# Performance work log

Hardware: AMD Instinct MI355X
Metric: run time of the kernel (lower is better)

## Reference

```python
import jax, jax.numpy as jnp
import numpy as np

N, DIM, HEADS, E = 20000, 256, 4, 100000
C = DIM  # TransformerConv out_channels per head (concat=False averages heads)


def setup_inputs() -> dict:
    key = jax.random.key(0)
    ks = jax.random.split(key, 12)
    s = DIM ** -0.5
    w = lambda k, shape: jax.random.normal(k, shape, jnp.float32) * s
    z = lambda shape: jnp.zeros(shape, jnp.float32)
    return {
        "f_all": jax.random.normal(ks[0], (N, DIM), jnp.float32),
        "edge_index": jax.random.randint(ks[1], (2, E), 0, N),
        "W_gcn": w(ks[2], (DIM, DIM)), "b_gcn": z((DIM,)),
        "W_q": w(ks[3], (DIM, HEADS * C)), "b_q": z((HEADS * C,)),
        "W_k": w(ks[4], (DIM, HEADS * C)), "b_k": z((HEADS * C,)),
        "W_v": w(ks[5], (DIM, HEADS * C)), "b_v": z((HEADS * C,)),
        "W_skip": w(ks[6], (DIM, DIM)), "b_skip": z((DIM,)),
        "W_beta": w(ks[7], (3 * DIM, 1)),
        "W_cnn": w(ks[8], (DIM, DIM)), "b_cnn": z((DIM,)),
    }


def reference(f_all, edge_index, W_gcn, b_gcn, W_q, b_q, W_k, b_k, W_v, b_v,
              W_skip, b_skip, W_beta, W_cnn, b_cnn):
    src, dst = edge_index[0], edge_index[1]

    # --- GCNConv: add self loops, symmetric D^-1/2 (A+I) D^-1/2 normalization ---
    loop = jnp.arange(N)
    s2 = jnp.concatenate([src, loop])
    d2 = jnp.concatenate([dst, loop])
    deg = jax.ops.segment_sum(jnp.ones_like(d2, jnp.float32), d2, N)
    dinv = jnp.where(deg > 0, 1.0 / jnp.sqrt(deg), 0.0)
    norm = dinv[s2] * dinv[d2]                    # [E+N]
    h = f_all @ W_gcn                             # [N, DIM]
    x = jax.ops.segment_sum(h[s2] * norm[:, None], d2, N) + b_gcn
    x = jax.nn.relu(x)

    # --- TransformerConv(heads=H, concat=False, beta=True) ---
    q = (x @ W_q + b_q).reshape(N, HEADS, C)
    k = (x @ W_k + b_k).reshape(N, HEADS, C)
    v = (x @ W_v + b_v).reshape(N, HEADS, C)
    logits = jnp.einsum('ehc,ehc->eh', q[dst], k[src]) / np.float32(np.sqrt(C))
    m = jax.ops.segment_max(logits, dst, N)       # per-target max for stable softmax
    e = jnp.exp(logits - m[dst])
    denom = jax.ops.segment_sum(e, dst, N)
    alpha = e / jnp.maximum(denom[dst], 1e-16)    # [E, H]
    agg = jax.ops.segment_sum(v[src] * alpha[:, :, None], dst, N)  # [N, H, C]
    out = agg.mean(axis=1)                        # concat=False -> head average
    xr = x @ W_skip + b_skip                      # root/skip branch
    beta = jax.nn.sigmoid(jnp.concatenate([out, xr, out - xr], axis=-1) @ W_beta)
    tf = jax.nn.relu(beta * xr + (1.0 - beta) * out)  # [N, DIM]

    # --- Conv1d with kernel (dim,1) on [1,1,dim,N]: per-node linear, output [dim,N] ---
    conv = jnp.einsum('cd,nd->cn', W_cnn, tf) + b_cnn[:, None]  # [DIM, N]
    # torch does .view(1, n_mole, -1) on the [1,dim,1,N] conv output: raw reshape
    return conv.reshape(1, N, DIM)
```

## Files before the change

### kernel.cpp

```cpp
#include <hip/hip_runtime.h>
#include <math.h>

#define DIMC 256
#define NHEAD 4
#define CAP 64

typedef unsigned short bf16u;
typedef __attribute__((ext_vector_type(8))) short bf16x8;
typedef __attribute__((ext_vector_type(4))) float f32x4;

typedef __attribute__((address_space(1))) const unsigned char ga_u8;
typedef __attribute__((address_space(3))) unsigned char lds_u8;
__device__ __forceinline__ void gld_lds16(const void* g, void* l) {
    __builtin_amdgcn_global_load_lds((ga_u8*)g, (lds_u8*)l, 16, 0, 0);
}

__device__ __forceinline__ float bf2f(bf16u u) {
    union { float f; unsigned int i; } c; c.i = ((unsigned int)u) << 16; return c.f;
}
__device__ __forceinline__ bf16u f2bf(float f) {
    union { float f; unsigned int i; } c; c.f = f;
    unsigned int r = c.i + 0x7fffu + ((c.i >> 16) & 1u);
    return (bf16u)(r >> 16);
}
__device__ __forceinline__ float4 load_bf4(const bf16u* p) {
    ushort4 raw = *(const ushort4*)p;
    return make_float4(bf2f(raw.x), bf2f(raw.y), bf2f(raw.z), bf2f(raw.w));
}
__device__ __forceinline__ void store_bf4(bf16u* p, float4 v) {
    ushort4 raw;
    raw.x = f2bf(v.x); raw.y = f2bf(v.y); raw.z = f2bf(v.z); raw.w = f2bf(v.w);
    *(ushort4*)p = raw;
}
__device__ __forceinline__ void load_bf8(const bf16u* p, float* o) {
    bf16x8 raw = *(const bf16x8*)p;
#pragma unroll
    for (int i = 0; i < 8; ++i) {
        union { float f; unsigned int u; } c;
        c.u = ((unsigned int)(unsigned short)raw[i]) << 16;
        o[i] = c.f;
    }
}
__device__ __forceinline__ void store_bf8(bf16u* p, const float* v) {
    bf16x8 raw;
#pragma unroll
    for (int i = 0; i < 8; ++i) raw[i] = (short)f2bf(v[i]);
    *(bf16x8*)p = raw;
}


__global__ void fill_kernel(const int* __restrict__ src, const int* __restrict__ dst,
                            int* __restrict__ cursor, int* __restrict__ srcs, int E) {
    int e = blockIdx.x * 256 + threadIdx.x;
    if (e < E) {
        int d = dst[e];
        int pos = atomicAdd(&cursor[d], 1);
        if (pos < CAP) srcs[d * CAP + pos] = src[e];
    }
}


__global__ __launch_bounds__(256) void prep_kernel(
    const float* __restrict__ f_all, int n4_f,
    const float* __restrict__ W_gcn, const float* __restrict__ W_q,
    const float* __restrict__ W_k, const float* __restrict__ W_v,
    const float* __restrict__ W_skip, const float* __restrict__ W_cnn,
    const float* __restrict__ b_q, const float* __restrict__ b_v,
    const float* __restrict__ b_skip,
    bf16u* __restrict__ xbuf, bf16u* __restrict__ WgcnT,
    bf16u* __restrict__ BTyp, bf16u* __restrict__ BT_vs,
    bf16u* __restrict__ A_wq, bf16u* __restrict__ A_wk,
    bf16u* __restrict__ Wcnn_b,
    float* __restrict__ ybias, float* __restrict__ bvm,
    int* __restrict__ cursor, int N) {
    __shared__ float T[32][33];
    int b = blockIdx.x, t = threadIdx.x;
    int nf = (n4_f + 255) >> 8;
    int nz = (N + 255) >> 8;
    if (b < nf) {
        int i = b * 256 + t;
        if (i < n4_f) {
            float4 vv = *(const float4*)(f_all + (size_t)i * 4);
            store_bf4(xbuf + (size_t)i * 4, vv);
        }
        return;
    }
    b -= nf;
    if (b < 64) {
        int i = b * 256 + t;
        float4 vv = *(const float4*)(W_cnn + (size_t)i * 4);
        store_bf4(Wcnn_b + (size_t)i * 4, vv);
        return;
    }
    b -= 64;
    if (b < 4) {
        int h = b, j = t;
        const float4* bq4 = (const float4*)(b_q + h * 256);
        const float4* wk4 = (const float4*)(W_k + (size_t)j * 1024 + h * 256);
        float acc = 0.f;
        for (int u = 0; u < 64; ++u) {
            float4 a = bq4[u], w = wk4[u];
            acc += a.x * w.x + a.y * w.y + a.z * w.z + a.w * w.w;
        }
        ybias[h * 256 + j] = acc;
        return;
    }
    b -= 4;
    if (b < 1) {
        ybias[1024 + t] = b_skip[t];
        bvm[t] = 0.25f * (b_v[t] + b_v[256 + t] + b_v[512 + t] + b_v[768 + t]);
        return;
    }
    b -= 1;
    if (b < nz) {
        int i = b * 256 + t;
        if (i < N) cursor[i] = 0;
        return;
    }
    b -= nz;
    if (b < 512) {
        const float* W = (b < 256) ? W_q : W_k;
        bf16u* out = (b < 256) ? A_wq : A_wk;
        int i4 = (b & 255) * 256 + t;
        int e = i4 * 4;
        int g = e >> 8, t4 = e & 255;
        float4 vv = *(const float4*)(W + (size_t)(g & 255) * 1024 + (g >> 8) * 256 + t4);
        store_bf4(out + (size_t)e, vv);
        return;
    }
    b -= 512;
    const float* src; bf16u* dst;
    int inld, inrow0, incol0, outld, outrow0, outcol0;
    if (b < 64) {
        int N0 = (b & 7) * 32, K0 = (b >> 3) * 32;
        src = W_gcn; inld = 256; inrow0 = K0; incol0 = N0;
        dst = WgcnT; outld = 256; outrow0 = N0; outcol0 = K0;
    } else if (b < 128) {
        int bb = b - 64; int N0 = (bb & 7) * 32, K0 = (bb >> 3) * 32;
        src = W_skip; inld = 256; inrow0 = K0; incol0 = N0;
        dst = BTyp;  outld = 256; outrow0 = 1024 + N0; outcol0 = K0;
    } else {
        int bb = b - 128; int jt = bb & 7, ct = (bb >> 3) & 7, hh = bb >> 6;
        src = W_v;  inld = 1024; inrow0 = ct * 32; incol0 = hh * 256 + jt * 32;
        dst = BT_vs; outld = 1024; outrow0 = jt * 32; outcol0 = hh * 256 + ct * 32;
    }
    int tx = t & 31, ty = t >> 5;
#pragma unroll
    for (int i = 0; i < 4; ++i)
        T[ty + 8 * i][tx] = src[(size_t)(inrow0 + ty + 8 * i) * inld + incol0 + tx];
    __syncthreads();
#pragma unroll
    for (int i = 0; i < 4; ++i)
        dst[(size_t)(outrow0 + ty + 8 * i) * outld + outcol0 + tx] = f2bf(T[tx][ty + 8 * i]);
}


template <bool ROWBIAS>
__global__ __launch_bounds__(256) void gemm_tile(const bf16u* __restrict__ A,
                                                 const bf16u* __restrict__ BT,
                                                 const float* __restrict__ bias,
                                                 void* __restrict__ Cout,
                                                 int M, int Nc, int ldc, int K,
                                                 int zstrA, int zstrB, int zstrC) {
    __shared__ __align__(16) bf16u As[2][128][32];
    __shared__ __align__(16) bf16u Bs[2][128][32];
    A += (size_t)blockIdx.z * zstrA;
    BT += (size_t)blockIdx.z * zstrB;
    int t = threadIdx.x;
    int w = t >> 6, lane = t & 63;
    int q = lane >> 4, r = lane & 15;
    int wm = (w & 1) * 64, wn = (w >> 1) * 64;
    int bm = blockIdx.y * 128, bn = blockIdx.x * 128;

    int srow = t >> 2, scol = (t & 3) * 8;
    int arow0 = bm + srow;      if (arow0 >= M)  arow0 = M - 1;
    int arow1 = bm + 64 + srow; if (arow1 >= M)  arow1 = M - 1;
    int brow0 = bn + srow;      if (brow0 >= Nc) brow0 = Nc - 1;
    int brow1 = bn + 64 + srow; if (brow1 >= Nc) brow1 = Nc - 1;
    const bf16u* a0 = A + (size_t)arow0 * K + scol;
    const bf16u* a1 = A + (size_t)arow1 * K + scol;
    const bf16u* b0 = BT + (size_t)brow0 * K + scol;
    const bf16u* b1 = BT + (size_t)brow1 * K + scol;

    char* As_base = (char*)&As[0][0][0] + w * 1024;
    char* Bs_base = (char*)&Bs[0][0][0] + w * 1024;

    f32x4 acc[4][4] = {};
    int ngroups = K >> 6;
    for (int g = 0; g < ngroups; ++g) {
        int k0 = g * 64;
        gld_lds16(a0 + k0, As_base);
        gld_lds16(a1 + k0, As_base + 4096);
        gld_lds16(b0 + k0, Bs_base);
        gld_lds16(b1 + k0, Bs_base + 4096);
        gld_lds16(a0 + k0 + 32, As_base + 8192);
        gld_lds16(a1 + k0 + 32, As_base + 8192 + 4096);
        gld_lds16(b0 + k0 + 32, Bs_base + 8192);
        gld_lds16(b1 + k0 + 32, Bs_base + 8192 + 4096);
        __syncthreads();
#pragma unroll
        for (int ks = 0; ks < 2; ++ks) {
            bf16x8 af[4], bfr[4];
#pragma unroll
            for (int i = 0; i < 4; ++i) af[i] = *(const bf16x8*)&As[ks][wm + i * 16 + r][q * 8];
#pragma unroll
            for (int j = 0; j < 4; ++j) bfr[j] = *(const bf16x8*)&Bs[ks][wn + j * 16 + r][q * 8];
#pragma unroll
            for (int i = 0; i < 4; ++i)
#pragma unroll
                for (int j = 0; j < 4; ++j)
                    acc[i][j] = __builtin_amdgcn_mfma_f32_16x16x32_bf16(af[i], bfr[j], acc[i][j], 0, 0, 0);
        }
        __syncthreads();
    }

    if (ROWBIAS) {
        float* C = (float*)Cout + (size_t)blockIdx.z * zstrC;
#pragma unroll
        for (int j = 0; j < 4; ++j) {
            int col = bn + wn + j * 16 + r;
            if (col >= Nc) continue;
#pragma unroll
            for (int i = 0; i < 4; ++i)
#pragma unroll
                for (int rg = 0; rg < 4; ++rg) {
                    int row = bm + wm + i * 16 + q * 4 + rg;
                    if (row < M)
                        __builtin_nontemporal_store(acc[i][j][rg] + bias[row],
                                                    &C[(size_t)row * ldc + col]);
                }
        }
    } else {
        __shared__ __align__(16) bf16u Cs[32][128];
        bf16u* C = (bf16u*)Cout + (size_t)blockIdx.z * zstrC;
        float cb4[4];
#pragma unroll
        for (int j = 0; j < 4; ++j) {
            int col = bn + wn + j * 16 + r;
            cb4[j] = bias ? bias[col] : 0.0f;
        }
        int rhalf = (w & 1) * 16;
        int colbase = (w >> 1) * 64;
        __syncthreads();
#pragma unroll
        for (int i = 0; i < 4; ++i) {
#pragma unroll
            for (int j = 0; j < 4; ++j)
#pragma unroll
                for (int rg = 0; rg < 4; ++rg)
                    Cs[rhalf + q * 4 + rg][colbase + j * 16 + r] = f2bf(acc[i][j][rg] + cb4[j]);
            __syncthreads();
#pragma unroll
            for (int cpass = 0; cpass < 2; ++cpass) {
                int chunk = cpass * 256 + t;
                int sr = chunk >> 4;
                int c16 = chunk & 15;
                int grow = bm + (sr < 16 ? i * 16 + sr : 64 + i * 16 + (sr - 16));
                if (grow < M)
                    __builtin_nontemporal_store(*(const bf16x8*)&Cs[sr][c16 * 8],
                                                (bf16x8*)&C[(size_t)grow * ldc + bn + c16 * 8]);
            }
            __syncthreads();
        }
    }
}


__global__ __launch_bounds__(256) void gcn_agg_kernel(const bf16u* __restrict__ h,
                                                      const int* __restrict__ cursor,
                                                      const int* __restrict__ srcs,
                                                      const float* __restrict__ b_gcn,
                                                      bf16u* __restrict__ x, int N) {
    int n = blockIdx.x * 8 + (threadIdx.x >> 5);
    if (n >= N) return;
    int lane = threadIdx.x & 31;
    int cb = lane * 8;
    int cnt = cursor[n]; if (cnt > CAP) cnt = CAP;
    float dn = rsqrtf((float)(cnt + 1));
    float hn[8];
    load_bf8(h + (size_t)n * DIMC + cb, hn);
    int base = n * CAP;
    float acc[8] = {};
    int i = 0;
    for (; i + 4 <= cnt; i += 4) {
        int4 s4 = *(const int4*)(srcs + base + i);
        float d0 = rsqrtf((float)(cursor[s4.x] + 1));
        float d1 = rsqrtf((float)(cursor[s4.y] + 1));
        float d2 = rsqrtf((float)(cursor[s4.z] + 1));
        float d3 = rsqrtf((float)(cursor[s4.w] + 1));
        float h0[8], h1[8], h2[8], h3[8];
        load_bf8(h + (size_t)s4.x * DIMC + cb, h0);
        load_bf8(h + (size_t)s4.y * DIMC + cb, h1);
        load_bf8(h + (size_t)s4.z * DIMC + cb, h2);
        load_bf8(h + (size_t)s4.w * DIMC + cb, h3);
#pragma unroll
        for (int j = 0; j < 8; ++j)
            acc[j] += h0[j] * d0 + h1[j] * d1 + h2[j] * d2 + h3[j] * d3;
    }
    for (; i < cnt; ++i) {
        int s = srcs[base + i];
        float ds = rsqrtf((float)(cursor[s] + 1));
        float hv[8];
        load_bf8(h + (size_t)s * DIMC + cb, hv);
#pragma unroll
        for (int j = 0; j < 8; ++j) acc[j] += hv[j] * ds;
    }
    float4 bg0 = *(const float4*)(b_gcn + cb);
    float4 bg1 = *(const float4*)(b_gcn + cb + 4);
    float bg[8] = {bg0.x, bg0.y, bg0.z, bg0.w, bg1.x, bg1.y, bg1.z, bg1.w};
    float dnn = dn * dn;
    float o[8];
#pragma unroll
    for (int j = 0; j < 8; ++j) o[j] = fmaxf(dn * acc[j] + hn[j] * dnn + bg[j], 0.f);
    store_bf8(x + (size_t)n * DIMC + cb, o);
}


__global__ __launch_bounds__(256) void attn_kernel(const bf16u* __restrict__ Y, int ldy,
                                                   const bf16u* __restrict__ x,
                                                   const int* __restrict__ cursor,
                                                   const int* __restrict__ srcs,
                                                   bf16u* __restrict__ Z, int N) {
    int n = blockIdx.x * 4 + (threadIdx.x >> 6);
    if (n >= N) return;
    int lane = threadIdx.x & 63;
    int hq = lane >> 4;
    int r = lane & 15;
    const float scale = 0.0625f;

    float yv[16];
    const bf16u* yrow = Y + (size_t)n * ldy + hq * DIMC + r * 16;
    load_bf8(yrow, yv);
    load_bf8(yrow + 8, yv + 8);
#pragma unroll
    for (int j = 0; j < 16; ++j) yv[j] *= scale;

    int cnt = cursor[n]; if (cnt > CAP) cnt = CAP;
    int base = n * CAP;
    float m = -INFINITY, denom = 0.f;
    float acc[16];
#pragma unroll
    for (int j = 0; j < 16; ++j) acc[j] = 0.f;

    int i = 0;
    for (; i + 2 <= cnt; i += 2) {
        int2 ss = *(const int2*)(srcs + base + i);
        const bf16u* x0p = x + (size_t)ss.x * DIMC + r * 16;
        const bf16u* x1p = x + (size_t)ss.y * DIMC + r * 16;
        float x0[16], x1[16];
        load_bf8(x0p, x0); load_bf8(x0p + 8, x0 + 8);
        load_bf8(x1p, x1); load_bf8(x1p + 8, x1 + 8);
        float d0 = 0.f, d1 = 0.f;
#pragma unroll
        for (int j = 0; j < 16; ++j) { d0 += yv[j] * x0[j]; d1 += yv[j] * x1[j]; }
#pragma unroll
        for (int msk = 1; msk <= 8; msk <<= 1) {
            d0 += __shfl_xor(d0, msk, 64);
            d1 += __shfl_xor(d1, msk, 64);
        }
        float nm = fmaxf(m, fmaxf(d0, d1));
        float so = __expf(m - nm);
        float p0 = __expf(d0 - nm);
        float p1 = __expf(d1 - nm);
        denom = denom * so + p0 + p1;
#pragma unroll
        for (int j = 0; j < 16; ++j) acc[j] = acc[j] * so + p0 * x0[j] + p1 * x1[j];
        m = nm;
    }
    if (i < cnt) {
        int s = srcs[base + i];
        const bf16u* xp = x + (size_t)s * DIMC + r * 16;
        float xs[16];
        load_bf8(xp, xs); load_bf8(xp + 8, xs + 8);
        float d = 0.f;
#pragma unroll
        for (int j = 0; j < 16; ++j) d += yv[j] * xs[j];
#pragma unroll
        for (int msk = 1; msk <= 8; msk <<= 1) d += __shfl_xor(d, msk, 64);
        float nm = fmaxf(m, d);
        float so = __expf(m - nm);
        float p = __expf(d - nm);
        denom = denom * so + p;
#pragma unroll
        for (int j = 0; j < 16; ++j) acc[j] = acc[j] * so + p * xs[j];
        m = nm;
    }

    float inv = 0.25f / fmaxf(denom, 1e-16f);
    float o[16];
#pragma unroll
    for (int j = 0; j < 16; ++j) o[j] = acc[j] * inv;
    bf16u* zrow = Z + (size_t)n * 1024 + hq * DIMC + r * 16;
    store_bf8(zrow, o);
    store_bf8(zrow + 8, o + 8);
}


__global__ __launch_bounds__(256) void beta_kernel(const bf16u* __restrict__ outz,
                                                   const bf16u* __restrict__ Yp, int ldy,
                                                   const float* __restrict__ bvm,
                                                   const float* __restrict__ W_beta,
                                                   const int* __restrict__ cursor,
                                                   bf16u* __restrict__ tf, int N) {
    int n = blockIdx.x * 8 + (threadIdx.x >> 5);
    if (n >= N) return;
    int lane = threadIdx.x & 31;
    int cb = lane * 8;
    float ov[8], xr[8];
    load_bf8(outz + (size_t)n * DIMC + cb, ov);
    load_bf8(Yp + (size_t)n * ldy + 1024 + cb, xr);
    float gate = (cursor[n] > 0) ? 1.f : 0.f;
#pragma unroll
    for (int j = 0; j < 8; ++j) ov[j] += gate * bvm[cb + j];
    float contrib = 0.f;
#pragma unroll
    for (int j = 0; j < 8; ++j) {
        float w1 = W_beta[cb + j];
        float w2 = W_beta[256 + cb + j];
        float w3 = W_beta[512 + cb + j];
        contrib += ov[j] * w1 + xr[j] * w2 + (ov[j] - xr[j]) * w3;
    }
#pragma unroll
    for (int msk = 1; msk <= 16; msk <<= 1) contrib += __shfl_xor(contrib, msk, 64);
    float beta = 1.0f / (1.0f + __expf(-contrib));
    float tv[8];
#pragma unroll
    for (int j = 0; j < 8; ++j) tv[j] = fmaxf(beta * xr[j] + (1.0f - beta) * ov[j], 0.f);
    store_bf8(tf + (size_t)n * DIMC + cb, tv);
}


static inline size_t align_up(size_t x) { return (x + 255) & ~(size_t)255; }

extern "C" void kernel_launch(void* const* d_in, const int* in_sizes, int n_in,
                              void* d_out, int out_size, void* d_ws, size_t ws_size,
                              hipStream_t stream) {
    const float* f_all  = (const float*)d_in[0];
    const int*   eidx   = (const int*)d_in[1];
    const float* W_gcn  = (const float*)d_in[2];
    const float* b_gcn  = (const float*)d_in[3];
    const float* W_q    = (const float*)d_in[4];
    const float* b_q    = (const float*)d_in[5];
    const float* W_k    = (const float*)d_in[6];
    const float* W_v    = (const float*)d_in[8];
    const float* b_v    = (const float*)d_in[9];
    const float* W_skip = (const float*)d_in[10];
    const float* b_skip = (const float*)d_in[11];
    const float* W_beta = (const float*)d_in[12];
    const float* W_cnn  = (const float*)d_in[13];
    const float* b_cnn  = (const float*)d_in[14];

    const int N = in_sizes[0] / DIMC;
    const int E = in_sizes[1] / 2;
    const int* src = eidx;
    const int* dst = eidx + E;

    char* p = (char*)d_ws;
    auto alloc = [&](size_t bytes) { char* r = p; p += align_up(bytes); return r; };
    int*   cursor = (int*)alloc((size_t)N * 4);
    int*   srcs   = (int*)alloc((size_t)N * CAP * 4);
    bf16u* WgcnT  = (bf16u*)alloc(256 * 256 * 2);
    bf16u* BTyp   = (bf16u*)alloc((size_t)1280 * 256 * 2);
    bf16u* BT_vs  = (bf16u*)alloc((size_t)256 * 1024 * 2);
    bf16u* A_wq   = (bf16u*)alloc((size_t)1024 * 256 * 2);
    bf16u* A_wk   = (bf16u*)alloc((size_t)1024 * 256 * 2);
    bf16u* Wcnn_b = (bf16u*)alloc(256 * 256 * 2);
    float* ybias  = (float*)alloc(1280 * 4);
    float* bvm    = (float*)alloc(256 * 4);
    bf16u* xbuf   = (bf16u*)alloc((size_t)N * DIMC * 2);
    bf16u* h      = (bf16u*)alloc((size_t)N * DIMC * 2);
    bf16u* Yp     = (bf16u*)alloc((size_t)N * 1280 * 2);
    bf16u* Z      = (bf16u*)alloc((size_t)N * 1024 * 2);
    bf16u* outz   = (bf16u*)alloc((size_t)N * DIMC * 2);

    int n4_f = N * DIMC / 4;
    int nf = (n4_f + 255) >> 8;
    int nz = (N + 255) >> 8;
    prep_kernel<<<nf + 64 + 4 + 1 + nz + 512 + 384, 256, 0, stream>>>(
        f_all, n4_f, W_gcn, W_q, W_k, W_v, W_skip, W_cnn,
        b_q, b_v, b_skip, xbuf, WgcnT, BTyp, BT_vs, A_wq, A_wk, Wcnn_b,
        ybias, bvm, cursor, N);

    fill_kernel<<<(E + 255) / 256, 256, 0, stream>>>(src, dst, cursor, srcs, E);

    gemm_tile<false><<<dim3(2, 2, 4), 256, 0, stream>>>(
        A_wk, A_wq, nullptr, BTyp, 256, 256, 256, 256, 65536, 65536, 65536);

    int mby = (N + 127) / 128;
    gemm_tile<false><<<dim3(2, mby), 256, 0, stream>>>(
        xbuf, WgcnT, nullptr, h, N, 256, 256, 256, 0, 0, 0);
    gcn_agg_kernel<<<(N + 7) / 8, 256, 0, stream>>>(h, cursor, srcs, b_gcn, xbuf, N);
    gemm_tile<false><<<dim3(10, mby), 256, 0, stream>>>(
        xbuf, BTyp, ybias, Yp, N, 1280, 1280, 256, 0, 0, 0);
    attn_kernel<<<(N + 3) / 4, 256, 0, stream>>>(Yp, 1280, xbuf, cursor, srcs, Z, N);
    gemm_tile<false><<<dim3(2, mby), 256, 0, stream>>>(
        Z, BT_vs, nullptr, outz, N, 256, 256, 1024, 0, 0, 0);
    beta_kernel<<<(N + 7) / 8, 256, 0, stream>>>(outz, Yp, 1280, bvm, W_beta, cursor, h, N);
    gemm_tile<true><<<dim3((N + 127) / 128, 2), 256, 0, stream>>>(
        Wcnn_b, h, b_cnn, (float*)d_out, 256, N, N, 256, 0, 0, 0);
}
```

Measured before the change: 253.7 us.

## Fuse Wk·Wqᵀ weight GEMM into prep kernel and unroll edge loops by four

The separate conversion of W_q/W_k to bf16 and the batched 256x256 weight-product GEMM launch are replaced by 16 extra blocks in prep_kernel. These blocks load fp32 weights, convert them in LDS, run MFMA and write the combined matrix directly, which removes one kernel launch and an intermediate buffer round trip. The GCN aggregation and attention edge loops are also restructured to process four neighbours per iteration with masked tails instead of a remainder loop, aiming for more memory-level parallelism per gather. Risks are higher register pressure in attn_kernel and a larger LDS footprint for every prep block.

New measurement: 262.3 us. 1.03x slower.

```diff
diff --git a/kernel.cpp b/kernel.cpp
--- a/kernel.cpp
+++ b/kernel.cpp
@@ -22,10 +22,6 @@
     union { float f; unsigned int i; } c; c.f = f;
     unsigned int r = c.i + 0x7fffu + ((c.i >> 16) & 1u);
     return (bf16u)(r >> 16);
-}
-__device__ __forceinline__ float4 load_bf4(const bf16u* p) {
-    ushort4 raw = *(const ushort4*)p;
-    return make_float4(bf2f(raw.x), bf2f(raw.y), bf2f(raw.z), bf2f(raw.w));
 }
 __device__ __forceinline__ void store_bf4(bf16u* p, float4 v) {
     ushort4 raw;
@@ -69,14 +65,90 @@
     const float* __restrict__ b_skip,
     bf16u* __restrict__ xbuf, bf16u* __restrict__ WgcnT,
     bf16u* __restrict__ BTyp, bf16u* __restrict__ BT_vs,
-    bf16u* __restrict__ A_wq, bf16u* __restrict__ A_wk,
     bf16u* __restrict__ Wcnn_b,
     float* __restrict__ ybias, float* __restrict__ bvm,
     int* __restrict__ cursor, int N) {
-    __shared__ float T[32][33];
+    __shared__ __align__(16) char sh[40960];
     int b = blockIdx.x, t = threadIdx.x;
     int nf = (n4_f + 255) >> 8;
     int nz = (N + 255) >> 8;
+
+    if (b < 16) {
+        bf16u (*As)[128][32] = (bf16u(*)[128][32])sh;
+        bf16u (*Bs)[128][32] = (bf16u(*)[128][32])(sh + 16384);
+        bf16u (*Cs)[128]     = (bf16u(*)[128])(sh + 32768);
+        int rb = b >> 1, cb = b & 1;
+        int h = rb >> 1;
+        int j0 = (rb & 1) * 128;
+        int t0 = h * 256;
+        int w = t >> 6, lane = t & 63;
+        int q = lane >> 4, r = lane & 15;
+        int wm = (w & 1) * 64, wn = (w >> 1) * 64;
+        int srow = t >> 2, scol = (t & 3) * 8;
+        const float* ak0 = W_k + (size_t)(j0 + srow) * 1024 + t0 + scol;
+        const float* ak1 = W_k + (size_t)(j0 + 64 + srow) * 1024 + t0 + scol;
+        const float* bq0 = W_q + (size_t)(cb * 128 + srow) * 1024 + t0 + scol;
+        const float* bq1 = W_q + (size_t)(cb * 128 + 64 + srow) * 1024 + t0 + scol;
+        auto stage = [&](const float* gp, bf16u* lp) {
+            float4 u = *(const float4*)gp, v = *(const float4*)(gp + 4);
+            bf16x8 o;
+            o[0] = (short)f2bf(u.x); o[1] = (short)f2bf(u.y);
+            o[2] = (short)f2bf(u.z); o[3] = (short)f2bf(u.w);
+            o[4] = (short)f2bf(v.x); o[5] = (short)f2bf(v.y);
+            o[6] = (short)f2bf(v.z); o[7] = (short)f2bf(v.w);
+            *(bf16x8*)lp = o;
+        };
+        f32x4 acc[4][4] = {};
+        for (int g = 0; g < 4; ++g) {
+            int k0 = g * 64;
+            stage(ak0 + k0,      &As[0][srow][scol]);
+            stage(ak1 + k0,      &As[0][64 + srow][scol]);
+            stage(ak0 + k0 + 32, &As[1][srow][scol]);
+            stage(ak1 + k0 + 32, &As[1][64 + srow][scol]);
+            stage(bq0 + k0,      &Bs[0][srow][scol]);
+            stage(bq1 + k0,      &Bs[0][64 + srow][scol]);
+            stage(bq0 + k0 + 32, &Bs[1][srow][scol]);
+            stage(bq1 + k0 + 32, &Bs[1][64 + srow][scol]);
+            __syncthreads();
+#pragma unroll
+            for (int ks = 0; ks < 2; ++ks) {
+                bf16x8 af[4], bfr[4];
+#pragma unroll
+                for (int i = 0; i < 4; ++i) af[i] = *(const bf16x8*)&As[ks][wm + i * 16 + r][q * 8];
+#pragma unroll
+                for (int j = 0; j < 4; ++j) bfr[j] = *(const bf16x8*)&Bs[ks][wn + j * 16 + r][q * 8];
+#pragma unroll
+                for (int i = 0; i < 4; ++i)
+#pragma unroll
+                    for (int j = 0; j < 4; ++j)
+                        acc[i][j] = __builtin_amdgcn_mfma_f32_16x16x32_bf16(af[i], bfr[j], acc[i][j], 0, 0, 0);
+            }
+            __syncthreads();
+        }
+        int bm = rb * 128, bn = cb * 128;
+        int rhalf = (w & 1) * 16;
+        int colbase = (w >> 1) * 64;
+#pragma unroll
+        for (int i = 0; i < 4; ++i) {
+#pragma unroll
+            for (int j = 0; j < 4; ++j)
+#pragma unroll
+                for (int rg = 0; rg < 4; ++rg)
+                    Cs[rhalf + q * 4 + rg][colbase + j * 16 + r] = f2bf(acc[i][j][rg]);
+            __syncthreads();
+#pragma unroll
+            for (int cpass = 0; cpass < 2; ++cpass) {
+                int chunk = cpass * 256 + t;
+                int sr = chunk >> 4;
+                int c16 = chunk & 15;
+                int grow = bm + (sr < 16 ? i * 16 + sr : 64 + i * 16 + (sr - 16));
+                *(bf16x8*)&BTyp[(size_t)grow * 256 + bn + c16 * 8] = *(const bf16x8*)&Cs[sr][c16 * 8];
+            }
+            __syncthreads();
+        }
+        return;
+    }
+    b -= 16;
     if (b < nf) {
         int i = b * 256 + t;
         if (i < n4_f) {
@@ -118,17 +190,7 @@
         return;
     }
     b -= nz;
-    if (b < 512) {
-        const float* W = (b < 256) ? W_q : W_k;
-        bf16u* out = (b < 256) ? A_wq : A_wk;
-        int i4 = (b & 255) * 256 + t;
-        int e = i4 * 4;
-        int g = e >> 8, t4 = e & 255;
-        float4 vv = *(const float4*)(W + (size_t)(g & 255) * 1024 + (g >> 8) * 256 + t4);
-        store_bf4(out + (size_t)e, vv);
-        return;
-    }
-    b -= 512;
+    float (*T)[33] = (float(*)[33])sh;
     const float* src; bf16u* dst;
     int inld, inrow0, incol0, outld, outrow0, outcol0;
     if (b < 64) {
@@ -160,12 +222,9 @@
                                                  const bf16u* __restrict__ BT,
                                                  const float* __restrict__ bias,
                                                  void* __restrict__ Cout,
-                                                 int M, int Nc, int ldc, int K,
-                                                 int zstrA, int zstrB, int zstrC) {
+                                                 int M, int Nc, int ldc, int K) {
     __shared__ __align__(16) bf16u As[2][128][32];
     __shared__ __align__(16) bf16u Bs[2][128][32];
-    A += (size_t)blockIdx.z * zstrA;
-    BT += (size_t)blockIdx.z * zstrB;
     int t = threadIdx.x;
     int w = t >> 6, lane = t & 63;
     int q = lane >> 4, r = lane & 15;
@@ -215,7 +274,7 @@
     }
 
     if (ROWBIAS) {
-        float* C = (float*)Cout + (size_t)blockIdx.z * zstrC;
+        float* C = (float*)Cout;
 #pragma unroll
         for (int j = 0; j < 4; ++j) {
             int col = bn + wn + j * 16 + r;
@@ -232,7 +291,7 @@
         }
     } else {
         __shared__ __align__(16) bf16u Cs[32][128];
-        bf16u* C = (bf16u*)Cout + (size_t)blockIdx.z * zstrC;
+        bf16u* C = (bf16u*)Cout;
         float cb4[4];
 #pragma unroll
         for (int j = 0; j < 4; ++j) {
@@ -281,29 +340,31 @@
     load_bf8(h + (size_t)n * DIMC + cb, hn);
     int base = n * CAP;
     float acc[8] = {};
-    int i = 0;
-    for (; i + 4 <= cnt; i += 4) {
-        int4 s4 = *(const int4*)(srcs + base + i);
-        float d0 = rsqrtf((float)(cursor[s4.x] + 1));
-        float d1 = rsqrtf((float)(cursor[s4.y] + 1));
-        float d2 = rsqrtf((float)(cursor[s4.z] + 1));
-        float d3 = rsqrtf((float)(cursor[s4.w] + 1));
+    int iters = (cnt + 3) >> 2;
+    for (int it = 0; it < iters; ++it) {
+        int e0 = it * 4, nv = cnt - e0;
+        int i0, i1, i2, i3;
+        if (nv >= 4) {
+            int4 s4 = *(const int4*)(srcs + base + e0);
+            i0 = s4.x; i1 = s4.y; i2 = s4.z; i3 = s4.w;
+        } else {
+            i0 = srcs[base + e0];
+            i1 = srcs[base + (nv > 1 ? e0 + 1 : e0)];
+            i2 = srcs[base + (nv > 2 ? e0 + 2 : e0)];
+            i3 = i2;
+        }
+        float d0 = rsqrtf((float)(cursor[i0] + 1));
+        float d1 = nv > 1 ? rsqrtf((float)(cursor[i1] + 1)) : 0.f;
+        float d2 = nv > 2 ? rsqrtf((float)(cursor[i2] + 1)) : 0.f;
+        float d3 = nv > 3 ? rsqrtf((float)(cursor[i3] + 1)) : 0.f;
         float h0[8], h1[8], h2[8], h3[8];
-        load_bf8(h + (size_t)s4.x * DIMC + cb, h0);
-        load_bf8(h + (size_t)s4.y * DIMC + cb, h1);
-        load_bf8(h + (size_t)s4.z * DIMC + cb, h2);
-        load_bf8(h + (size_t)s4.w * DIMC + cb, h3);
+        load_bf8(h + (size_t)i0 * DIMC + cb, h0);
+        load_bf8(h + (size_t)i1 * DIMC + cb, h1);
+        load_bf8(h + (size_t)i2 * DIMC + cb, h2);
+        load_bf8(h + (size_t)i3 * DIMC + cb, h3);
 #pragma unroll
         for (int j = 0; j < 8; ++j)
-            acc[j] += h0[j] * d0 + h1[j] * d1 + h2[j] * d2 + h3[j] * d3;
-    }
-    for (; i < cnt; ++i) {
-        int s = srcs[base + i];
-        float ds = rsqrtf((float)(cursor[s] + 1));
-        float hv[8];
-        load_bf8(h + (size_t)s * DIMC + cb, hv);
-#pragma unroll
-        for (int j = 0; j < 8; ++j) acc[j] += hv[j] * ds;
+            acc[j] += (h0[j] * d0 + h1[j] * d1) + (h2[j] * d2 + h3[j] * d3);
     }
     float4 bg0 = *(const float4*)(b_gcn + cb);
     float4 bg1 = *(const float4*)(b_gcn + cb + 4);
@@ -342,47 +403,51 @@
 #pragma unroll
     for (int j = 0; j < 16; ++j) acc[j] = 0.f;
 
-    int i = 0;
-    for (; i + 2 <= cnt; i += 2) {
-        int2 ss = *(const int2*)(srcs + base + i);
-        const bf16u* x0p = x + (size_t)ss.x * DIMC + r * 16;
-        const bf16u* x1p = x + (size_t)ss.y * DIMC + r * 16;
-        float x0[16], x1[16];
-        load_bf8(x0p, x0); load_bf8(x0p + 8, x0 + 8);
-        load_bf8(x1p, x1); load_bf8(x1p + 8, x1 + 8);
-        float d0 = 0.f, d1 = 0.f;
-#pragma unroll
-        for (int j = 0; j < 16; ++j) { d0 += yv[j] * x0[j]; d1 += yv[j] * x1[j]; }
+    int iters = (cnt + 3) >> 2;
+    for (int it = 0; it < iters; ++it) {
+        int e0 = it * 4, nv = cnt - e0;
+        int i0, i1, i2, i3;
+        if (nv >= 4) {
+            int4 s4 = *(const int4*)(srcs + base + e0);
+            i0 = s4.x; i1 = s4.y; i2 = s4.z; i3 = s4.w;
+        } else {
+            i0 = srcs[base + e0];
+            i1 = srcs[base + (nv > 1 ? e0 + 1 : e0)];
+            i2 = srcs[base + (nv > 2 ? e0 + 2 : e0)];
+            i3 = i2;
+        }
+        const bf16u* p0 = x + (size_t)i0 * DIMC + r * 16;
+        const bf16u* p1 = x + (size_t)i1 * DIMC + r * 16;
+        const bf16u* p2 = x + (size_t)i2 * DIMC + r * 16;
+        const bf16u* p3 = x + (size_t)i3 * DIMC + r * 16;
+        float x0[16], x1[16], x2[16], x3[16];
+        load_bf8(p0, x0); load_bf8(p0 + 8, x0 + 8);
+        load_bf8(p1, x1); load_bf8(p1 + 8, x1 + 8);
+        load_bf8(p2, x2); load_bf8(p2 + 8, x2 + 8);
+        load_bf8(p3, x3); load_bf8(p3 + 8, x3 + 8);
+        float d0 = 0.f, d1 = 0.f, d2 = 0.f, d3 = 0.f;
+#pragma unroll
+        for (int j = 0; j < 16; ++j) {
+            d0 += yv[j] * x0[j]; d1 += yv[j] * x1[j];
+            d2 += yv[j] * x2[j]; d3 += yv[j] * x3[j];
+        }
 #pragma unroll
         for (int msk = 1; msk <= 8; msk <<= 1) {
-            d0 += __shfl_xor(d0, msk, 64);
-            d1 += __shfl_xor(d1, msk, 64);
-        }
-        float nm = fmaxf(m, fmaxf(d0, d1));
+            d0 += __shfl_xor(d0, msk, 64); d1 += __shfl_xor(d1, msk, 64);
+            d2 += __shfl_xor(d2, msk, 64); d3 += __shfl_xor(d3, msk, 64);
+        }
+        if (nv < 2) d1 = -INFINITY;
+        if (nv < 3) d2 = -INFINITY;
+        if (nv < 4) d3 = -INFINITY;
+        float mx = fmaxf(fmaxf(d0, d1), fmaxf(d2, d3));
+        float nm = fmaxf(m, mx);
         float so = __expf(m - nm);
-        float p0 = __expf(d0 - nm);
-        float p1 = __expf(d1 - nm);
-        denom = denom * so + p0 + p1;
-#pragma unroll
-        for (int j = 0; j < 16; ++j) acc[j] = acc[j] * so + p0 * x0[j] + p1 * x1[j];
-        m = nm;
-    }
-    if (i < cnt) {
-        int s = srcs[base + i];
-        const bf16u* xp = x + (size_t)s * DIMC + r * 16;
-        float xs[16];
-        load_bf8(xp, xs); load_bf8(xp + 8, xs + 8);
-        float d = 0.f;
-#pragma unroll
-        for (int j = 0; j < 16; ++j) d += yv[j] * xs[j];
-#pragma unroll
-        for (int msk = 1; msk <= 8; msk <<= 1) d += __shfl_xor(d, msk, 64);
-        float nm = fmaxf(m, d);
-        float so = __expf(m - nm);
-        float p = __expf(d - nm);
-        denom = denom * so + p;
-#pragma unroll
-        for (int j = 0; j < 16; ++j) acc[j] = acc[j] * so + p * xs[j];
+        float e0p = __expf(d0 - nm), e1p = __expf(d1 - nm);
+        float e2p = __expf(d2 - nm), e3p = __expf(d3 - nm);
+        denom = denom * so + (e0p + e1p) + (e2p + e3p);
+#pragma unroll
+        for (int j = 0; j < 16; ++j)
+            acc[j] = acc[j] * so + (e0p * x0[j] + e1p * x1[j]) + (e2p * x2[j] + e3p * x3[j]);
         m = nm;
     }
 
@@ -462,8 +527,6 @@
     bf16u* WgcnT  = (bf16u*)alloc(256 * 256 * 2);
     bf16u* BTyp   = (bf16u*)alloc((size_t)1280 * 256 * 2);
     bf16u* BT_vs  = (bf16u*)alloc((size_t)256 * 1024 * 2);
-    bf16u* A_wq   = (bf16u*)alloc((size_t)1024 * 256 * 2);
-    bf16u* A_wk   = (bf16u*)alloc((size_t)1024 * 256 * 2);
     bf16u* Wcnn_b = (bf16u*)alloc(256 * 256 * 2);
     float* ybias  = (float*)alloc(1280 * 4);
     float* bvm    = (float*)alloc(256 * 4);
@@ -476,26 +539,20 @@
     int n4_f = N * DIMC / 4;
     int nf = (n4_f + 255) >> 8;
     int nz = (N + 255) >> 8;
-    prep_kernel<<<nf + 64 + 4 + 1 + nz + 512 + 384, 256, 0, stream>>>(
+    prep_kernel<<<16 + nf + 64 + 4 + 1 + nz + 384, 256, 0, stream>>>(
         f_all, n4_f, W_gcn, W_q, W_k, W_v, W_skip, W_cnn,
-        b_q, b_v, b_skip, xbuf, WgcnT, BTyp, BT_vs, A_wq, A_wk, Wcnn_b,
+        b_q, b_v, b_skip, xbuf, WgcnT, BTyp, BT_vs, Wcnn_b,
         ybias, bvm, cursor, N);
 
     fill_kernel<<<(E + 255) / 256, 256, 0, stream>>>(src, dst, cursor, srcs, E);
 
-    gemm_tile<false><<<dim3(2, 2, 4), 256, 0, stream>>>(
-        A_wk, A_wq, nullptr, BTyp, 256, 256, 256, 256, 65536, 65536, 65536);
-
     int mby = (N + 127) / 128;
-    gemm_tile<false><<<dim3(2, mby), 256, 0, stream>>>(
-        xbuf, WgcnT, nullptr, h, N, 256, 256, 256, 0, 0, 0);
+    gemm_tile<false><<<dim3(2, mby), 256, 0, stream>>>(xbuf, WgcnT, nullptr, h, N, 256, 256, 256);
     gcn_agg_kernel<<<(N + 7) / 8, 256, 0, stream>>>(h, cursor, srcs, b_gcn, xbuf, N);
-    gemm_tile<false><<<dim3(10, mby), 256, 0, stream>>>(
-        xbuf, BTyp, ybias, Yp, N, 1280, 1280, 256, 0, 0, 0);
+    gemm_tile<false><<<dim3(10, mby), 256, 0, stream>>>(xbuf, BTyp, ybias, Yp, N, 1280, 1280, 256);
     attn_kernel<<<(N + 3) / 4, 256, 0, stream>>>(Yp, 1280, xbuf, cursor, srcs, Z, N);
-    gemm_tile<false><<<dim3(2, mby), 256, 0, stream>>>(
-        Z, BT_vs, nullptr, outz, N, 256, 256, 1024, 0, 0, 0);
+    gemm_tile<false><<<dim3(2, mby), 256, 0, stream>>>(Z, BT_vs, nullptr, outz, N, 256, 256, 1024);
     beta_kernel<<<(N + 7) / 8, 256, 0, stream>>>(outz, Yp, 1280, bvm, W_beta, cursor, h, N);
     gemm_tile<true><<<dim3((N + 127) / 128, 2), 256, 0, stream>>>(
-        Wcnn_b, h, b_cnn, (float*)d_out, 256, N, N, 256, 0, 0, 0);
-}
+        Wcnn_b, h, b_cnn, (float*)d_out, 256, N, N, 256);
+}
```
